# Optimization experiments

Measured on AMD Instinct MI355X. Metric: run time of the kernel, lower is better.

Reference implementation:

```python
import jax, jax.numpy as jnp
import numpy as np

HID, H, C, L = 128, 4, 128, 3  # hidden, heads, per-head out (concat=False -> mean over heads), layers
OUT = 256
N_HEX, N_VERT, N_EDGE, B = 19, 54, 72, 1024
F_HEX, F_VERT, F_EDGE, F_PLY = 9, 7, 5, 14


def _topology():
    # Deterministic stand-in for the Catan board topology (same edge counts as the env).
    rng = np.random.RandomState(0)
    hv = rng.randint(0, N_VERT, size=(N_HEX, 6))            # each hex touches 6 vertices
    v0 = rng.randint(0, N_VERT, size=N_EDGE)                # board-edge endpoints
    v1 = (v0 + 1 + rng.randint(0, N_VERT - 1, size=N_EDGE)) % N_VERT
    h_src = np.repeat(np.arange(N_HEX), 6); h_dst = hv.reshape(-1)           # 114 edges
    e_src = np.repeat(np.arange(N_EDGE), 2); e_dst = np.stack([v0, v1], 1).reshape(-1)  # 144
    vv_s = np.concatenate([v0, v1]); vv_d = np.concatenate([v1, v0])          # 144
    # (src_idx, dst_idx, n_dst) per relation, order matches RELATION_TYPES
    rels = [(h_src, h_dst, N_VERT),   # hex -> vertex
            (h_dst, h_src, N_HEX),    # vertex -> hex
            (e_dst, e_src, N_EDGE),   # vertex -> edge
            (e_src, e_dst, N_VERT),   # edge -> vertex
            (vv_s, vv_d, N_VERT)]     # vertex -> vertex
    return [(jnp.asarray(s, jnp.int32), jnp.asarray(d, jnp.int32), nd) for s, d, nd in rels]

RELS = _topology()
REL_TYPES = [("hex", "vertex"), ("vertex", "hex"), ("vertex", "edge"), ("edge", "vertex"), ("vertex", "vertex")]
NODE_TYPES = ("hex", "vertex", "edge")


def _gat(x_src, x_dst, W, a_s, a_d, b, src, dst, n_dst):
    """PyG GATConv (heads=H, concat=False, add_self_loops=False, shared lin)."""
    bsz = x_src.shape[0]
    g = (x_src @ W).reshape(bsz, -1, H, C)    # [B,Ns,H,C]
    gd = (x_dst @ W).reshape(bsz, -1, H, C)   # [B,Nd,H,C]
    es = jnp.einsum('bnhc,hc->bnh', g, a_s)
    ed = jnp.einsum('bnhc,hc->bnh', gd, a_d)
    e = jax.nn.leaky_relu(es[:, src] + ed[:, dst], 0.2)   # [B,E,H]
    e = jnp.transpose(e, (1, 0, 2))                       # [E,B,H]
    m = jax.ops.segment_max(e, dst, num_segments=n_dst)   # per-dst softmax
    ex = jnp.exp(e - m[dst])
    s = jax.ops.segment_sum(ex, dst, num_segments=n_dst)
    alpha = ex / (s[dst] + 1e-16)
    msg = jnp.transpose(g, (1, 0, 2, 3))[src] * alpha[..., None]   # [E,B,H,C]
    out = jax.ops.segment_sum(msg, dst, num_segments=n_dst)       # [Nd,B,H,C]
    return jnp.transpose(out.mean(axis=2), (1, 0, 2)) + b         # mean over heads, + bias


def _ln(x, g, b):
    mu = x.mean(-1, keepdims=True)
    var = ((x - mu) ** 2).mean(-1, keepdims=True)
    return (x - mu) / jnp.sqrt(var + 1e-5) * g + b


def setup_inputs() -> dict:
    key = jax.random.key(0)
    ks = jax.random.split(key, 20)
    rn = lambda k, shape, s=0.05: jax.random.normal(k, shape, jnp.float32) * s
    pool_dim = 3 * HID + F_PLY
    return {
        'hex_features': rn(ks[0], (B, N_HEX, F_HEX), 1.0),
        'vertex_features': rn(ks[1], (B, N_VERT, F_VERT), 1.0),
        'edge_features': rn(ks[2], (B, N_EDGE, F_EDGE), 1.0),
        'player_features': rn(ks[3], (B, 4, F_PLY), 1.0),
        'in_hexW': rn(ks[4], (F_HEX, HID)), 'in_hexb': jnp.zeros((HID,), jnp.float32),
        'in_vertW': rn(ks[5], (F_VERT, HID)), 'in_vertb': jnp.zeros((HID,), jnp.float32),
        'in_edgeW': rn(ks[6], (F_EDGE, HID)), 'in_edgeb': jnp.zeros((HID,), jnp.float32),
        'gat_W': rn(ks[7], (L, 5, HID, H * C)),
        'gat_asrc': rn(ks[8], (L, 5, H, C)),
        'gat_adst': rn(ks[9], (L, 5, H, C)),
        'gat_b': jnp.zeros((L, 5, C), jnp.float32),
        'ln_g': jnp.ones((L, 3, HID), jnp.float32),
        'ln_b': jnp.zeros((L, 3, HID), jnp.float32),
        'mlp_W1': rn(ks[10], (pool_dim, HID)), 'mlp_b1': jnp.zeros((HID,), jnp.float32),
        'mlp_W2': rn(ks[11], (HID, OUT)), 'mlp_b2': jnp.zeros((OUT,), jnp.float32),
        'current_player': jax.random.randint(ks[12], (B,), 0, 4, jnp.int32),
    }


def reference(hex_features, vertex_features, edge_features, player_features,
              in_hexW, in_hexb, in_vertW, in_vertb, in_edgeW, in_edgeb,
              gat_W, gat_asrc, gat_adst, gat_b, ln_g, ln_b,
              mlp_W1, mlp_b1, mlp_W2, mlp_b2, current_player):
    x = {'hex': hex_features @ in_hexW + in_hexb,
         'vertex': vertex_features @ in_vertW + in_vertb,
         'edge': edge_features @ in_edgeW + in_edgeb}
    for l in range(L):
        agg = {nt: jnp.zeros_like(x[nt]) for nt in NODE_TYPES}
        for r, (st, dt) in enumerate(REL_TYPES):
            src, dst, n_dst = RELS[r]
            agg[dt] = agg[dt] + _gat(x[st], x[dt], gat_W[l, r], gat_asrc[l, r],
                                     gat_adst[l, r], gat_b[l, r], src, dst, n_dst)
        for i, nt in enumerate(NODE_TYPES):
            x[nt] = jax.nn.relu(_ln(agg[nt] + x[nt], ln_g[l, i], ln_b[l, i]))
    pools = [x[nt].mean(axis=1) for nt in NODE_TYPES]  # mean-pool each node type
    cur = jnp.take_along_axis(player_features, current_player[:, None, None], axis=1)[:, 0]
    feat = jnp.concatenate(pools + [cur], axis=-1)     # [B, 3*HID + F_PLY]
    h = jax.nn.relu(feat @ mlp_W1 + mlp_b1)
    return h @ mlp_W2 + mlp_b2
```

## Files before the change

kernel.cpp:

```cpp
#include <hip/hip_runtime.h>
#include <math.h>

#define NB 1024
#define NHEX 19
#define NVERT 54
#define NEDGE 72
#define NNODE 145
#define HID 128
#define NLAYERS 3
#define MAXE 144
#define OUTD 256
#define FPLY 14
#define POOLD 398
#define ESD_PB 5120

typedef unsigned short ushort_t;
typedef short bf16x8 __attribute__((ext_vector_type(8)));
typedef float f32x4 __attribute__((ext_vector_type(4)));
typedef float f32x2 __attribute__((ext_vector_type(2)));

static __device__ __forceinline__ float bf2f(ushort_t u) {
    return __uint_as_float(((unsigned int)u) << 16);
}
static __device__ __forceinline__ ushort_t f2bf(float f) {
    unsigned int u = __float_as_uint(f);
    return (ushort_t)((u + 0x7fffu + ((u >> 16) & 1u)) >> 16);
}
static __device__ __forceinline__ unsigned pk2(float lo, float hi) {
    unsigned r;
    asm("v_cvt_pk_bf16_f32 %0, %1, %2" : "=v"(r) : "v"(lo), "v"(hi));
    return r;
}
static __device__ __forceinline__ float blo(unsigned u) { return __uint_as_float(u << 16); }
static __device__ __forceinline__ float bhi(unsigned u) { return __uint_as_float(u & 0xffff0000u); }
static __device__ __forceinline__ f32x4 MF(uint4 a, uint4 b, f32x4 c) {
    return __builtin_amdgcn_mfma_f32_16x16x32_bf16(
        __builtin_bit_cast(bf16x8, a), __builtin_bit_cast(bf16x8, b), c, 0, 0, 0);
}
static __device__ __forceinline__ int xba(int row, int cb) {
    return (row * 256 + cb) ^ ((row & 7) << 4);
}

__device__ void topo_body(char* sm, int* __restrict__ cst_g, unsigned* __restrict__ pck_g) {
    unsigned* mt = (unsigned*)(sm);
    int* t6   = (int*)(sm + 2496);
    int* sc   = (int*)(sm + 4992);
    int* hv   = (int*)(sm + 7488);
    int* v0a  = (int*)(sm + 7944);
    int* v1a  = (int*)(sm + 8232);
    int* cnt  = (int*)(sm + 8520);
    int* cnt0 = (int*)(sm + 8840);
    int* stt  = (int*)(sm + 9160);
    int* J186 = (int*)(sm + 9480);
    int* M    = (int*)(sm + 9488);
    const int tid = threadIdx.x;

    if (tid == 0) {
        unsigned s = 0u;
        for (int i = 0; i < 624; ++i) { mt[i] = s; s = 1812433253u * (s ^ (s >> 30)) + (unsigned)i + 1u; }
    }
    __syncthreads();
    {
        unsigned a = 0, bb = 0, c = 0;
        if (tid < 227) { a = mt[tid]; bb = mt[tid + 1]; c = mt[tid + 397]; }
        __syncthreads();
        if (tid < 227) {
            unsigned y = (a & 0x80000000u) | (bb & 0x7fffffffu);
            mt[tid] = c ^ (y >> 1) ^ ((bb & 1u) ? 0x9908b0dfu : 0u);
        }
        __syncthreads();
    }
    {
        int i = 227 + tid;
        unsigned a = 0, bb = 0, c = 0;
        if (tid < 227) { a = mt[i]; bb = mt[i + 1]; c = mt[i - 227]; }
        __syncthreads();
        if (tid < 227) {
            unsigned y = (a & 0x80000000u) | (bb & 0x7fffffffu);
            mt[i] = c ^ (y >> 1) ^ ((bb & 1u) ? 0x9908b0dfu : 0u);
        }
        __syncthreads();
    }
    {
        int i = 454 + tid;
        unsigned a = 0, bb = 0, c = 0;
        if (tid < 170) { a = mt[i]; bb = mt[(i + 1) % 624]; c = mt[i - 227]; }
        __syncthreads();
        if (tid < 170) {
            unsigned y = (a & 0x80000000u) | (bb & 0x7fffffffu);
            mt[i] = c ^ (y >> 1) ^ ((bb & 1u) ? 0x9908b0dfu : 0u);
        }
        __syncthreads();
    }
    for (int i = tid; i < 624; i += 256) {
        unsigned y = mt[i];
        y ^= y >> 11; y ^= (y << 7) & 0x9d2c5680u; y ^= (y << 15) & 0xefc60000u; y ^= y >> 18;
        t6[i] = (int)(y & 63u);
    }
    __syncthreads();
#define SCAN624()                                                          \
    for (int off = 1; off < 624; off <<= 1) {                              \
        int v0_ = 0, v1_ = 0, v2_ = 0;                                     \
        int i0 = tid, i1 = tid + 256, i2 = tid + 512;                      \
        if (i0 >= off) v0_ = sc[i0 - off];                                 \
        if (i1 >= off) v1_ = sc[i1 - off];                                 \
        if (i2 < 624 && i2 >= off) v2_ = sc[i2 - off];                     \
        __syncthreads();                                                   \
        sc[i0] += v0_; sc[i1] += v1_;                                      \
        if (i2 < 624) sc[i2] += v2_;                                       \
        __syncthreads();                                                   \
    }
    for (int i = tid; i < 624; i += 256) sc[i] = (t6[i] <= 53) ? 1 : 0;
    __syncthreads();
    SCAN624();
    for (int i = tid; i < 624; i += 256) {
        if (t6[i] <= 53) {
            int k = sc[i];
            if (k <= 114) hv[k - 1] = t6[i];
            else if (k <= 186) v0a[k - 115] = t6[i];
            if (k == 186) *J186 = i;
        }
    }
    __syncthreads();
    int Jcap = *J186;
    for (int i = tid; i < 624; i += 256) sc[i] = (i > Jcap && t6[i] <= 52) ? 1 : 0;
    __syncthreads();
    SCAN624();
    for (int i = tid; i < 624; i += 256) {
        if (i > Jcap && t6[i] <= 52) {
            int k = sc[i];
            if (k <= 72) v1a[k - 1] = (v0a[k - 1] + 1 + t6[i]) % 54;
        }
    }
    __syncthreads();
#undef SCAN624
    const int En[5]  = {114, 114, 144, 144, 144};
    const int Ndn[5] = {54, 19, 72, 54, 54};
    const int Nsn[5] = {19, 54, 54, 72, 54};
    for (int r = 0; r < 5; ++r) {
        const int E = En[r], Nd = Ndn[r], Ns = Nsn[r];
        const int tot = Nd * Ns;
        for (int i = tid; i < tot; i += 256) M[i] = 0;
        __syncthreads();
        for (int k = tid; k < E; k += 256) {
            int s, d;
            if (r == 0)      { s = k / 6; d = hv[k]; }
            else if (r == 1) { s = hv[k]; d = k / 6; }
            else if (r == 2) { s = (k & 1) ? v1a[k >> 1] : v0a[k >> 1]; d = k >> 1; }
            else if (r == 3) { s = k >> 1; d = (k & 1) ? v1a[k >> 1] : v0a[k >> 1]; }
            else             { s = (k < 72) ? v0a[k] : v1a[k - 72]; d = (k < 72) ? v1a[k] : v0a[k - 72]; }
            atomicAdd(&M[d * Ns + s], 1);
        }
        __syncthreads();
        if (tid < Nd) {
            int c = 0;
            const int base = tid * Ns;
            for (int s = 0; s < Ns; ++s) c += (M[base + s] != 0) ? 1 : 0;
            cnt[tid] = c;
            cnt0[tid] = c;
        }
        __syncthreads();
        for (int off = 1; off < 128; off <<= 1) {
            int v = 0;
            if (tid < Nd && tid >= off) v = cnt[tid - off];
            __syncthreads();
            if (tid < Nd && tid >= off) cnt[tid] += v;
            __syncthreads();
        }
        if (tid < Nd) {
            int st = cnt[tid] - cnt0[tid];
            stt[tid] = st;
            cst_g[r * 73 + tid] = st;
            if (tid == Nd - 1) cst_g[r * 73 + Nd] = cnt[tid];
        }
        __syncthreads();
        for (int i = tid; i < tot; i += 256) {
            int m = M[i];
            if (m > 0) {
                int d = i / Ns, s = i - d * Ns;
                int rank = 0;
                const int base = d * Ns;
                for (int s2 = 0; s2 < s; ++s2) rank += (M[base + s2] != 0) ? 1 : 0;
                pck_g[r * 144 + stt[d] + rank] = (unsigned)(s | (d << 8) | (m << 16));
            }
        }
        __syncthreads();
    }
}

__device__ void wvec_body(char* sm, int lr, const float* __restrict__ gat_W,
                          const float* __restrict__ gat_asrc,
                          const float* __restrict__ gat_adst,
                          ushort_t* __restrict__ wvb) {
    float* as_s = (float*)(sm);
    float* ad_s = (float*)(sm + 2048);
    int tid = threadIdx.x;
    for (int i = tid; i < 512; i += 256) {
        as_s[i] = gat_asrc[(size_t)lr * 512 + i];
        ad_s[i] = gat_adst[(size_t)lr * 512 + i];
    }
    __syncthreads();
    ushort_t* wb = wvb + (size_t)lr * 2048;
    const float* W = gat_W + (size_t)lr * 128 * 512;
    int t127 = tid & 127, rhalf = tid >> 7;
    int h = t127 >> 5, c4 = t127 & 31;
    for (int k0 = 0; k0 < 128; k0 += 2) {
        int k = k0 + rhalf;
        float4 wv4 = *(const float4*)(W + (size_t)k * 512 + h * 128 + c4 * 4);
        const float* a = as_s + h * 128 + c4 * 4;
        const float* dd = ad_s + h * 128 + c4 * 4;
        float pa = wv4.x * a[0] + wv4.y * a[1] + wv4.z * a[2] + wv4.w * a[3];
        float pd = wv4.x * dd[0] + wv4.y * dd[1] + wv4.z * dd[2] + wv4.w * dd[3];
        for (int m = 1; m < 32; m <<= 1) { pa += __shfl_xor(pa, m, 64); pd += __shfl_xor(pd, m, 64); }
        if (c4 == 0) {
            ushort_t pah = f2bf(pa), pdh = f2bf(pd);
            ushort_t pal = f2bf(pa - bf2f(pah)), pdl = f2bf(pd - bf2f(pdh));
            wb[h * 128 + k] = pah;        wb[(4 + h) * 128 + k] = pdh;
            wb[(8 + h) * 128 + k] = pal;  wb[(12 + h) * 128 + k] = pdl;
        }
    }
}

__device__ void wp_body(char* sm, int lrh, const float* __restrict__ gat_W, ushort_t* __restrict__ Wp) {
    ushort_t* tr = (ushort_t*)(sm);
    int lr = lrh >> 2, h = lrh & 3;
    const float* Wsrc = gat_W + (size_t)lr * 128 * 512 + h * 128;
    ushort_t* dst = Wp + (size_t)lrh * 128 * 128;
    for (int half = 0; half < 2; ++half) {
        for (int i = threadIdx.x; i < 128 * 16; i += 256) {
            int k = i >> 4, q2 = i & 15;
            float4 v = *(const float4*)(Wsrc + (size_t)k * 512 + half * 64 + q2 * 4);
            int nl = q2 * 4;
            tr[(nl + 0) * 130 + k] = f2bf(v.x);
            tr[(nl + 1) * 130 + k] = f2bf(v.y);
            tr[(nl + 2) * 130 + k] = f2bf(v.z);
            tr[(nl + 3) * 130 + k] = f2bf(v.w);
        }
        __syncthreads();
        for (int i = threadIdx.x; i < 64 * 16; i += 256) {
            int nl = i >> 4, q = i & 15;
            const ushort_t* s = tr + nl * 130 + q * 8;
            uint4 o;
            o.x = (unsigned)s[0] | ((unsigned)s[1] << 16);
            o.y = (unsigned)s[2] | ((unsigned)s[3] << 16);
            o.z = (unsigned)s[4] | ((unsigned)s[5] << 16);
            o.w = (unsigned)s[6] | ((unsigned)s[7] << 16);
            *(uint4*)(dst + (half * 64 + nl) * 128 + q * 8) = o;
        }
        __syncthreads();
    }
}

__global__ __launch_bounds__(256) void k_preA(
        int* __restrict__ cst_g, unsigned* __restrict__ pck_g,
        const float* __restrict__ gatW, const float* __restrict__ gatas,
        const float* __restrict__ gatad, ushort_t* __restrict__ wvb, ushort_t* __restrict__ Wp) {
    extern __shared__ char smem_dyn[];
    unsigned kb = blockIdx.x;
    if (kb == 0)      topo_body(smem_dyn, cst_g, pck_g);
    else if (kb < 16) wvec_body(smem_dyn, (int)kb - 1, gatW, gatas, gatad, wvb);
    else              wp_body(smem_dyn, (int)kb - 16, gatW, Wp);
}
#define PREA_SMEM 25088

__global__ __launch_bounds__(256) void k_projlog(
        const float* __restrict__ hexf, const float* __restrict__ vertf,
        const float* __restrict__ edgef,
        const float* __restrict__ Wh, const float* __restrict__ bh,
        const float* __restrict__ Wv, const float* __restrict__ bv,
        const float* __restrict__ We, const float* __restrict__ be,
        ushort_t* __restrict__ xb, const ushort_t* __restrict__ wvb,
        float* __restrict__ esd_g) {
    extern __shared__ char smem_dyn[];
    char*  smem = smem_dyn;
    float* Wl = (float*)(smem + 37120);
    float* bl = (float*)(smem + 48384);
    int b = blockIdx.x, tid = threadIdx.x, lane = tid & 63, wid = tid >> 6;
    const int kc16 = (lane >> 4) * 16;

    for (int i = tid; i < 9 * 128; i += 256) Wl[i] = Wh[i];
    for (int i = tid; i < 7 * 128; i += 256) Wl[9 * 128 + i] = Wv[i];
    for (int i = tid; i < 5 * 128; i += 256) Wl[16 * 128 + i] = We[i];
    if (tid < 128) { bl[tid] = bh[tid]; bl[128 + tid] = bv[tid]; bl[256 + tid] = be[tid]; }
    __syncthreads();
    int c = tid & 127;
    for (int n = tid >> 7; n < NNODE; n += 2) {
        const float* f; const float* W; const float* bias; int K;
        if (n < NHEX)              { f = hexf  + ((size_t)b * NHEX  + n) * 9;                  W = Wl;            bias = bl;       K = 9; }
        else if (n < NHEX + NVERT) { f = vertf + ((size_t)b * NVERT + (n - NHEX)) * 7;         W = Wl + 9 * 128;  bias = bl + 128; K = 7; }
        else                       { f = edgef + ((size_t)b * NEDGE + (n - NHEX - NVERT)) * 5; W = Wl + 16 * 128; bias = bl + 256; K = 5; }
        float acc = bias[c];
        for (int k = 0; k < K; ++k) acc += f[k] * W[k * 128 + c];
        ushort_t u = f2bf(acc);
        xb[((size_t)b * NNODE + n) * HID + c] = u;
        *(ushort_t*)(smem + xba(n, c * 2)) = u;
    }
    __syncthreads();

    const int NsA[5] = {19, 54, 54, 72, 54}, SbA[5] = {0, 19, 19, 73, 19};
    const int NdA[5] = {54, 19, 72, 54, 54}, DbA[5] = {19, 0, 73, 19, 19};
    for (int r = 0; r < 5; ++r) {
        int Ns = NsA[r];
        int RL = (r == 4) ? 54 : Ns + NdA[r];
        const ushort_t* wv = wvb + (size_t)r * 2048;
        uint4 bw[4];
#pragma unroll
        for (int ks = 0; ks < 4; ++ks)
            bw[ks] = *(const uint4*)(wv + (lane & 15) * 128 + ks * 32 + (lane >> 4) * 8);
        int T = (RL + 15) >> 4;
        for (int t = wid; t < T; t += 4) {
            int vrow = t * 16 + (lane & 15);
            int node = vrow < Ns ? SbA[r] + vrow : (vrow < RL ? DbA[r] + (vrow - Ns) : SbA[r]);
            f32x4 e = (f32x4){0.f, 0.f, 0.f, 0.f};
#pragma unroll
            for (int ks = 0; ks < 4; ++ks)
                e = MF(*(const uint4*)(smem + xba(node, ks * 64 + kc16)), bw[ks], e);
#pragma unroll
            for (int g = 0; g < 4; ++g) {
                float sv = e[g] + __shfl_xor(e[g], 8, 64);
                int row = t * 16 + (lane >> 4) * 4 + g;
                if ((lane & 15) < 8 && row < RL)
                    esd_g[(size_t)b * ESD_PB + r * 1024 + row * 8 + (lane & 15)] = sv;
            }
        }
    }
}
#define PROJLOG_SMEM 49920

template<int KIND>
__device__ __forceinline__ void gnn_body(char* smem, int b, int half,
        const ushort_t* __restrict__ xb_cur, ushort_t* __restrict__ xb_nxt,
        const float* __restrict__ esd_cur, float* __restrict__ esd_nxt,
        const int* __restrict__ cst_all, const unsigned* __restrict__ pck_all,
        const ushort_t* __restrict__ wvb, const ushort_t* __restrict__ Wp_g,
        const float* __restrict__ gatb_g,
        const float* __restrict__ lg, const float* __restrict__ lb, int l) {
    constexpr int ND    = (KIND == 0 ? 19 : KIND == 1 ? 36 : 54);
    constexpr int DBASE = (KIND == 0 ? 0 : KIND == 1 ? 73 : 19);
    constexpr int NSMAX = (KIND == 2 ? 72 : 54);
    constexpr int NRELF = (KIND == 2 ? 3 : 1);
    constexpr int MT    = (ND + 15) / 16;
    constexpr int O_Y   = NSMAX * 256;
    constexpr int O_ESD = O_Y + ND * 256;
    constexpr int O_AL  = O_ESD + 4064;
    constexpr int O_CST = O_AL + 2304;
    constexpr int O_PCK = O_CST + 304;

    constexpr int NS_A[3][3] = {{54, 0, 0}, {54, 0, 0}, {19, 72, 54}};
    constexpr int SB_A[3][3] = {{19, 0, 0}, {19, 0, 0}, {0, 73, 19}};
    constexpr int RR_A[3][3] = {{1, 0, 0}, {2, 0, 0}, {0, 3, 4}};
    constexpr int NRE = (KIND == 2 ? 5 : 2);
    constexpr int RE_R[3][5] = {{0, 1, 0, 0, 0}, {2, 3, 0, 0, 0}, {0, 1, 2, 3, 4}};
    constexpr int RE_B[3][5] = {{0, 54, 0, 0, 0}, {54, 0, 0, 0, 0}, {19, 0, 0, 72, 0}};

    float*    esdL = (float*)(smem + O_ESD);
    float*    alph = (float*)(smem + O_AL);
    int*      cstL = (int*)(smem + O_CST);
    unsigned* pckL = (unsigned*)(smem + O_PCK);

    const int tid = threadIdx.x, lane = tid & 63, wid = tid >> 6;
    const int nr0 = wid * 32 + (lane & 15);
    const int kc16 = (lane >> 4) * 16;
    const int d0 = half * ND;
    const int DB = DBASE + d0;
    const ushort_t* xcb = xb_cur + (size_t)b * NNODE * HID;

    f32x4 acc[MT][2];
#pragma unroll
    for (int mt = 0; mt < MT; ++mt) {
        acc[mt][0] = (f32x4){0.f, 0.f, 0.f, 0.f};
        acc[mt][1] = (f32x4){0.f, 0.f, 0.f, 0.f};
    }

#pragma unroll
    for (int ri = 0; ri < NRELF; ++ri) {
        const int NS = NS_A[KIND][ri], SBG = SB_A[KIND][ri], r = RR_A[KIND][ri];
        const bool SELF = (KIND == 2 && ri == 2);
        const int lr = l * 5 + r;
        const int ER = SELF ? ND : NS + ND;
        const int jlo = cst_all[r * 73 + d0];

        for (int i = tid; i < NS * 16; i += 256) {
            int row = i >> 4, q = i & 15;
            uint4 o = *(const uint4*)(xcb + (size_t)(SBG + row) * HID + q * 8);
            *(uint4*)(smem + xba(row, q * 16)) = o;
        }
        {
            const float* eg = esd_cur + (size_t)b * ESD_PB + (size_t)r * 1024;
            for (int i = tid; i < ER * 2; i += 256) {
                int row = i >> 1;
                int grow = (SELF || row < NS) ? row : row + d0;
                ((uint4*)esdL)[i] = ((const uint4*)eg)[grow * 2 + (i & 1)];
            }
        }
        for (int i = tid; i <= ND; i += 256) cstL[i] = cst_all[r * 73 + d0 + i] - jlo;
        for (int i = tid; jlo + i < 144; i += 256) pckL[i] = pck_all[r * 144 + jlo + i];
        __syncthreads();

        for (int i = tid; i < ND * 4; i += 256) {
            int d = i >> 2, h = i & 3;
            int s0 = cstL[d], s1 = cstL[d + 1];
            if (s0 == s1) continue;
            float edv = esdL[((SELF ? d + d0 : NS + d)) * 8 + 4 + h];
            float m = -1e30f;
            for (int j = s0; j < s1; ++j) {
                float sv = esdL[(pckL[j] & 255) * 8 + h] + edv;
                sv = (sv >= 0.f) ? sv : 0.2f * sv;
                alph[j * 4 + h] = sv;
                m = fmaxf(m, sv);
            }
            float sum = 0.f;
            for (int j = s0; j < s1; ++j) {
                float e = (float)(pckL[j] >> 16) * __expf(alph[j * 4 + h] - m);
                alph[j * 4 + h] = e;
                sum += e;
            }
            float inv = 1.f / (sum + 1e-16f);
            for (int j = s0; j < s1; ++j) alph[j * 4 + h] *= inv;
        }
        __syncthreads();

        for (int h = 0; h < 4; ++h) {
            for (int i = tid; i < ND * 16; i += 256) {
                int d = i >> 4, c8 = i & 15;
                int s0 = cstL[d], s1 = cstL[d + 1];
                f32x2 a01 = (f32x2){0.f, 0.f}, a23 = (f32x2){0.f, 0.f};
                f32x2 a45 = (f32x2){0.f, 0.f}, a67 = (f32x2){0.f, 0.f};
                for (int j = s0; j < s1; ++j) {
                    float al = alph[j * 4 + h];
                    f32x2 al2 = (f32x2){al, al};
                    uint4 xv = *(const uint4*)(smem + xba((int)(pckL[j] & 255), c8 * 16));
                    a01 += al2 * (f32x2){blo(xv.x), bhi(xv.x)};
                    a23 += al2 * (f32x2){blo(xv.y), bhi(xv.y)};
                    a45 += al2 * (f32x2){blo(xv.z), bhi(xv.z)};
                    a67 += al2 * (f32x2){blo(xv.w), bhi(xv.w)};
                }
                uint4 o;
                o.x = pk2(a01[0], a01[1]); o.y = pk2(a23[0], a23[1]);
                o.z = pk2(a45[0], a45[1]); o.w = pk2(a67[0], a67[1]);
                *(uint4*)(smem + O_Y + xba(d, c8 * 16)) = o;
            }
            const ushort_t* wpH = Wp_g + (size_t)(lr * 4 + h) * 16384;
            __syncthreads();
#pragma unroll
            for (int ks = 0; ks < 4; ++ks) {
                uint4 b0 = *(const uint4*)(wpH + (size_t)nr0 * 128 + ks * 32 + (lane >> 4) * 8);
                uint4 b1 = *(const uint4*)(wpH + (size_t)(nr0 + 16) * 128 + ks * 32 + (lane >> 4) * 8);
#pragma unroll
                for (int mt = 0; mt < MT; ++mt) {
                    int arow = mt * 16 + (lane & 15);
                    if (arow >= ND) arow = ND - 1;
                    uint4 av = *(const uint4*)(smem + O_Y + xba(arow, ks * 64 + kc16));
                    acc[mt][0] = MF(av, b0, acc[mt][0]);
                    acc[mt][1] = MF(av, b1, acc[mt][1]);
                }
            }
            __syncthreads();
        }
    }

    float bn0 = 0.f, bn1 = 0.f;
#pragma unroll
    for (int ri = 0; ri < NRELF; ++ri) {
        const float* bb = gatb_g + (size_t)(l * 5 + RR_A[KIND][ri]) * 128;
        bn0 += bb[nr0]; bn1 += bb[nr0 + 16];
    }
    const float lgc0 = lg[nr0], lgc1 = lg[nr0 + 16];
    const float lbc0 = lb[nr0], lbc1 = lb[nr0 + 16];
#pragma unroll
    for (int mt = 0; mt < MT; ++mt)
#pragma unroll
        for (int g = 0; g < 4; ++g) {
            int row = mt * 16 + (lane >> 4) * 4 + g;
            if (row < ND) {
                acc[mt][0][g] = 0.25f * acc[mt][0][g] + bn0 + bf2f(xcb[(size_t)(DB + row) * HID + nr0]);
                acc[mt][1][g] = 0.25f * acc[mt][1][g] + bn1 + bf2f(xcb[(size_t)(DB + row) * HID + nr0 + 16]);
            }
        }
    float* red1 = esdL;
    float* red2 = esdL + 320;
#pragma unroll
    for (int mt = 0; mt < MT; ++mt)
#pragma unroll
        for (int g = 0; g < 4; ++g) {
            float p = acc[mt][0][g] + acc[mt][1][g];
            for (int m = 1; m < 16; m <<= 1) p += __shfl_xor(p, m, 64);
            int row = mt * 16 + (lane >> 4) * 4 + g;
            if ((lane & 15) == 0 && row < ND) red1[row * 4 + wid] = p;
        }
    __syncthreads();
#pragma unroll
    for (int mt = 0; mt < MT; ++mt)
#pragma unroll
        for (int g = 0; g < 4; ++g) {
            int row = mt * 16 + (lane >> 4) * 4 + g;
            float mu = 0.f;
            if (row < ND)
                mu = (red1[row * 4] + red1[row * 4 + 1] + red1[row * 4 + 2] + red1[row * 4 + 3]) * (1.f / 128.f);
            acc[mt][0][g] -= mu;
            acc[mt][1][g] -= mu;
            float p = acc[mt][0][g] * acc[mt][0][g] + acc[mt][1][g] * acc[mt][1][g];
            for (int m = 1; m < 16; m <<= 1) p += __shfl_xor(p, m, 64);
            if ((lane & 15) == 0 && row < ND) red2[row * 4 + wid] = p;
        }
    __syncthreads();
#pragma unroll
    for (int mt = 0; mt < MT; ++mt)
#pragma unroll
        for (int g = 0; g < 4; ++g) {
            int row = mt * 16 + (lane >> 4) * 4 + g;
            if (row < ND) {
                float var = (red2[row * 4] + red2[row * 4 + 1] + red2[row * 4 + 2] + red2[row * 4 + 3]) * (1.f / 128.f);
                float rs = rsqrtf(var + 1e-5f);
                float o0 = fmaxf(acc[mt][0][g] * rs * lgc0 + lbc0, 0.f);
                float o1 = fmaxf(acc[mt][1][g] * rs * lgc1 + lbc1, 0.f);
                size_t gi = ((size_t)b * NNODE + DB + row) * HID;
                ushort_t u0 = f2bf(o0), u1 = f2bf(o1);
                xb_nxt[gi + nr0] = u0;
                xb_nxt[gi + nr0 + 16] = u1;
                if (esd_nxt) {
                    *(ushort_t*)(smem + O_Y + xba(row, nr0 * 2)) = u0;
                    *(ushort_t*)(smem + O_Y + xba(row, (nr0 + 16) * 2)) = u1;
                }
            }
        }
    if (esd_nxt) {
        __syncthreads();
        const int T = (ND + 15) >> 4;
        for (int t5 = wid; t5 < NRE * T; t5 += 4) {
            int e = t5 / T, tt = t5 % T;
            int r2 = RE_R[KIND][e], base = RE_B[KIND][e] + d0;
            const ushort_t* wv = wvb + (size_t)((l + 1) * 5 + r2) * 2048;
            uint4 bw[4];
#pragma unroll
            for (int ks = 0; ks < 4; ++ks)
                bw[ks] = *(const uint4*)(wv + (lane & 15) * 128 + ks * 32 + (lane >> 4) * 8);
            int arow = tt * 16 + (lane & 15);
            if (arow >= ND) arow = ND - 1;
            f32x4 ev = (f32x4){0.f, 0.f, 0.f, 0.f};
#pragma unroll
            for (int ks = 0; ks < 4; ++ks)
                ev = MF(*(const uint4*)(smem + O_Y + xba(arow, ks * 64 + kc16)), bw[ks], ev);
#pragma unroll
            for (int g = 0; g < 4; ++g) {
                float sv = ev[g] + __shfl_xor(ev[g], 8, 64);
                int row = tt * 16 + (lane >> 4) * 4 + g;
                if ((lane & 15) < 8 && row < ND)
                    esd_nxt[(size_t)b * ESD_PB + r2 * 1024 + (base + row) * 8 + (lane & 15)] = sv;
            }
        }
    }
}

#define SMEM_TOT 39504

__global__ __launch_bounds__(256, 4) void k_layer(
        const ushort_t* __restrict__ xb_cur, ushort_t* __restrict__ xb_nxt,
        const float* __restrict__ esd_cur, float* __restrict__ esd_nxt,
        const int* __restrict__ cst, const unsigned* __restrict__ pck,
        const ushort_t* __restrict__ wvb, const ushort_t* __restrict__ Wp,
        const float* __restrict__ gatb, const float* __restrict__ lngp,
        const float* __restrict__ lnbp, int l) {
    extern __shared__ uint4 smem_u4[];
    char* smem = (char*)smem_u4;
    unsigned kb = blockIdx.x;
    if (kb < NB)
        gnn_body<2>(smem, (int)kb, 0, xb_cur, xb_nxt, esd_cur, esd_nxt, cst, pck, wvb, Wp, gatb,
                    lngp + (size_t)(l * 3 + 1) * 128, lnbp + (size_t)(l * 3 + 1) * 128, l);
    else if (kb < 3 * NB) {
        unsigned t = kb - NB;
        gnn_body<1>(smem, (int)(t >> 1), (int)(t & 1), xb_cur, xb_nxt, esd_cur, esd_nxt, cst, pck, wvb, Wp, gatb,
                    lngp + (size_t)(l * 3 + 2) * 128, lnbp + (size_t)(l * 3 + 2) * 128, l);
    } else
        gnn_body<0>(smem, (int)(kb - 3 * NB), 0, xb_cur, xb_nxt, esd_cur, esd_nxt, cst, pck, wvb, Wp, gatb,
                    lngp + (size_t)(l * 3 + 0) * 128, lnbp + (size_t)(l * 3 + 0) * 128, l);
}

__global__ __launch_bounds__(256) void k_head(const ushort_t* __restrict__ xb, const float* __restrict__ playerf,
                                              const int* __restrict__ curp,
                                              const float* __restrict__ W1, const float* __restrict__ b1,
                                              const float* __restrict__ W2, const float* __restrict__ b2,
                                              float* __restrict__ out) {
    __shared__ float fs[POOLD];
    __shared__ float ps[256];
    __shared__ float h1s[HID];
    int b = blockIdx.x, t = threadIdx.x;
    int c = t & 127, half = t >> 7;
    const ushort_t* xbb = xb + (size_t)b * NNODE * HID;
    float s0 = 0.f, s1 = 0.f, s2 = 0.f;
    for (int n = half; n < NHEX; n += 2)                    s0 += bf2f(xbb[n * HID + c]);
    for (int n = NHEX + half; n < NHEX + NVERT; n += 2)     s1 += bf2f(xbb[n * HID + c]);
    for (int n = NHEX + NVERT + half; n < NNODE; n += 2)    s2 += bf2f(xbb[n * HID + c]);
    ps[t] = s0; __syncthreads();
    if (half == 0) fs[c] = (ps[c] + ps[128 + c]) * (1.f / 19.f);
    __syncthreads(); ps[t] = s1; __syncthreads();
    if (half == 0) fs[128 + c] = (ps[c] + ps[128 + c]) * (1.f / 54.f);
    __syncthreads(); ps[t] = s2; __syncthreads();
    if (half == 0) fs[256 + c] = (ps[c] + ps[128 + c]) * (1.f / 72.f);
    if (t < FPLY) fs[384 + t] = playerf[((size_t)b * 4 + curp[b]) * FPLY + t];
    __syncthreads();
    float a = 0.f;
    int k0 = half * 199, k1 = half ? POOLD : 199;
    for (int k = k0; k < k1; ++k) a += fs[k] * W1[(size_t)k * HID + c];
    ps[t] = a; __syncthreads();
    if (half == 0) h1s[c] = fmaxf(b1[c] + ps[c] + ps[128 + c], 0.f);
    __syncthreads();
    float o = b2[t];
    for (int j = 0; j < HID; ++j) o += h1s[j] * W2[(size_t)j * OUTD + t];
    out[(size_t)b * OUTD + t] = o;
}

static constexpr size_t alignUp(size_t v) { return (v + 255) & ~(size_t)255; }
static constexpr size_t OFF_CST  = 0;
static constexpr size_t OFF_PCK  = alignUp(OFF_CST + 5 * 73 * 4);
static constexpr size_t OFF_WVB  = alignUp(OFF_PCK + 5 * 144 * 4);
static constexpr size_t OFF_WP   = alignUp(OFF_WVB + (size_t)15 * 16 * 128 * 2);
static constexpr size_t OFF_XA   = alignUp(OFF_WP + (size_t)15 * 4 * 128 * 128 * 2);
static constexpr size_t OFF_XB2  = alignUp(OFF_XA + (size_t)NB * NNODE * HID * 2);
static constexpr size_t OFF_ESD0 = alignUp(OFF_XB2 + (size_t)NB * NNODE * HID * 2);
static constexpr size_t OFF_ESD1 = alignUp(OFF_ESD0 + (size_t)NB * ESD_PB * 4);

extern "C" void kernel_launch(void* const* d_in, const int* in_sizes, int n_in,
                              void* d_out, int out_size, void* d_ws, size_t ws_size,
                              hipStream_t stream) {
    (void)in_sizes; (void)n_in; (void)out_size; (void)ws_size;
    const float* hexf   = (const float*)d_in[0];
    const float* vertf  = (const float*)d_in[1];
    const float* edgef  = (const float*)d_in[2];
    const float* playerf= (const float*)d_in[3];
    const float* inhW   = (const float*)d_in[4];
    const float* inhb   = (const float*)d_in[5];
    const float* invW   = (const float*)d_in[6];
    const float* invb   = (const float*)d_in[7];
    const float* ineW   = (const float*)d_in[8];
    const float* ineb   = (const float*)d_in[9];
    const float* gatW   = (const float*)d_in[10];
    const float* gatas  = (const float*)d_in[11];
    const float* gatad  = (const float*)d_in[12];
    const float* gatb   = (const float*)d_in[13];
    const float* lngp   = (const float*)d_in[14];
    const float* lnbp   = (const float*)d_in[15];
    const float* mW1    = (const float*)d_in[16];
    const float* mb1    = (const float*)d_in[17];
    const float* mW2    = (const float*)d_in[18];
    const float* mb2    = (const float*)d_in[19];
    const int*   curp   = (const int*)d_in[20];
    float* out = (float*)d_out;

    char* ws = (char*)d_ws;
    int* cst        = (int*)(ws + OFF_CST);
    unsigned* pck   = (unsigned*)(ws + OFF_PCK);
    ushort_t* wvb   = (ushort_t*)(ws + OFF_WVB);
    ushort_t* Wp    = (ushort_t*)(ws + OFF_WP);
    ushort_t* xbA   = (ushort_t*)(ws + OFF_XA);
    ushort_t* xbB   = (ushort_t*)(ws + OFF_XB2);
    float* esd0     = (float*)(ws + OFF_ESD0);
    float* esd1     = (float*)(ws + OFF_ESD1);

    k_preA<<<76, 256, PREA_SMEM, stream>>>(cst, pck, gatW, gatas, gatad, wvb, Wp);
    k_projlog<<<NB, 256, PROJLOG_SMEM, stream>>>(hexf, vertf, edgef, inhW, inhb, invW, invb,
                                                 ineW, ineb, xbA, wvb, esd0);

    for (int l = 0; l < NLAYERS; ++l) {
        const ushort_t* cur = (l & 1) ? xbB : xbA;
        ushort_t* nxt = (l & 1) ? xbA : xbB;
        const float* ecur = (l & 1) ? esd1 : esd0;
        float* enxt = (l == 2) ? nullptr : ((l & 1) ? esd0 : esd1);
        k_layer<<<4 * NB, 256, SMEM_TOT, stream>>>(cur, nxt, ecur, enxt, cst, pck, wvb, Wp,
                                                   gatb, lngp, lnbp, l);
    }

    k_head<<<NB, 256, 0, stream>>>(xbB, playerf, curp, mW1, mb1, mW2, mb2, out);
}
```

Baseline: 779.9 us.

## Split vertex blocks in half and process two attention heads per pass

Vertex-destination work is split across two blocks of 27 nodes each, growing the grid from 4*NB to 5*NB blocks. The head loop now aggregates two heads per pass into two Y buffers, halving the number of syncthreads and aggregation passes while doubling the MFMA work per pass. Launch bounds drop from 4 to 2 waves per SIMD, which gives the extra accumulators more registers but may lower occupancy. The shared-memory layout grows because of the second Y buffer. The self-relation ESD row count changes to NS so that all 54 source rows are loaded.

```diff
diff --git a/kernel.cpp b/kernel.cpp
--- a/kernel.cpp
+++ b/kernel.cpp
@@ -335,13 +335,14 @@
         const ushort_t* __restrict__ wvb, const ushort_t* __restrict__ Wp_g,
         const float* __restrict__ gatb_g,
         const float* __restrict__ lg, const float* __restrict__ lb, int l) {
-    constexpr int ND    = (KIND == 0 ? 19 : KIND == 1 ? 36 : 54);
+    constexpr int ND    = (KIND == 0 ? 19 : KIND == 1 ? 36 : 27);
     constexpr int DBASE = (KIND == 0 ? 0 : KIND == 1 ? 73 : 19);
     constexpr int NSMAX = (KIND == 2 ? 72 : 54);
     constexpr int NRELF = (KIND == 2 ? 3 : 1);
     constexpr int MT    = (ND + 15) / 16;
     constexpr int O_Y   = NSMAX * 256;
-    constexpr int O_ESD = O_Y + ND * 256;
+    constexpr int YB1   = ND * 256;
+    constexpr int O_ESD = O_Y + 2 * ND * 256;
     constexpr int O_AL  = O_ESD + 4064;
     constexpr int O_CST = O_AL + 2304;
     constexpr int O_PCK = O_CST + 304;
@@ -377,7 +378,7 @@
         const int NS = NS_A[KIND][ri], SBG = SB_A[KIND][ri], r = RR_A[KIND][ri];
         const bool SELF = (KIND == 2 && ri == 2);
         const int lr = l * 5 + r;
-        const int ER = SELF ? ND : NS + ND;
+        const int ER = SELF ? NS : NS + ND;
         const int jlo = cst_all[r * 73 + d0];
 
         for (int i = tid; i < NS * 16; i += 256) {
@@ -420,39 +421,57 @@
         }
         __syncthreads();
 
-        for (int h = 0; h < 4; ++h) {
+#pragma unroll
+        for (int hp = 0; hp < 2; ++hp) {
+            const int h0 = hp * 2;
             for (int i = tid; i < ND * 16; i += 256) {
                 int d = i >> 4, c8 = i & 15;
                 int s0 = cstL[d], s1 = cstL[d + 1];
-                f32x2 a01 = (f32x2){0.f, 0.f}, a23 = (f32x2){0.f, 0.f};
-                f32x2 a45 = (f32x2){0.f, 0.f}, a67 = (f32x2){0.f, 0.f};
+                f32x2 y0a = (f32x2){0.f, 0.f}, y0b = (f32x2){0.f, 0.f};
+                f32x2 y0c = (f32x2){0.f, 0.f}, y0d = (f32x2){0.f, 0.f};
+                f32x2 y1a = (f32x2){0.f, 0.f}, y1b = (f32x2){0.f, 0.f};
+                f32x2 y1c = (f32x2){0.f, 0.f}, y1d = (f32x2){0.f, 0.f};
                 for (int j = s0; j < s1; ++j) {
-                    float al = alph[j * 4 + h];
-                    f32x2 al2 = (f32x2){al, al};
+                    float al0 = alph[j * 4 + h0];
+                    float al1 = alph[j * 4 + h0 + 1];
+                    f32x2 v0 = (f32x2){al0, al0}, v1 = (f32x2){al1, al1};
                     uint4 xv = *(const uint4*)(smem + xba((int)(pckL[j] & 255), c8 * 16));
-                    a01 += al2 * (f32x2){blo(xv.x), bhi(xv.x)};
-                    a23 += al2 * (f32x2){blo(xv.y), bhi(xv.y)};
-                    a45 += al2 * (f32x2){blo(xv.z), bhi(xv.z)};
-                    a67 += al2 * (f32x2){blo(xv.w), bhi(xv.w)};
+                    f32x2 e0 = (f32x2){blo(xv.x), bhi(xv.x)};
+                    f32x2 e1 = (f32x2){blo(xv.y), bhi(xv.y)};
+                    f32x2 e2 = (f32x2){blo(xv.z), bhi(xv.z)};
+                    f32x2 e3 = (f32x2){blo(xv.w), bhi(xv.w)};
+                    y0a += v0 * e0; y0b += v0 * e1; y0c += v0 * e2; y0d += v0 * e3;
+                    y1a += v1 * e0; y1b += v1 * e1; y1c += v1 * e2; y1d += v1 * e3;
                 }
-                uint4 o;
-                o.x = pk2(a01[0], a01[1]); o.y = pk2(a23[0], a23[1]);
-                o.z = pk2(a45[0], a45[1]); o.w = pk2(a67[0], a67[1]);
-                *(uint4*)(smem + O_Y + xba(d, c8 * 16)) = o;
-            }
-            const ushort_t* wpH = Wp_g + (size_t)(lr * 4 + h) * 16384;
+                uint4 o0, o1;
+                o0.x = pk2(y0a[0], y0a[1]); o0.y = pk2(y0b[0], y0b[1]);
+                o0.z = pk2(y0c[0], y0c[1]); o0.w = pk2(y0d[0], y0d[1]);
+                o1.x = pk2(y1a[0], y1a[1]); o1.y = pk2(y1b[0], y1b[1]);
+                o1.z = pk2(y1c[0], y1c[1]); o1.w = pk2(y1d[0], y1d[1]);
+                int ba = xba(d, c8 * 16);
+                *(uint4*)(smem + O_Y + ba) = o0;
+                *(uint4*)(smem + O_Y + YB1 + ba) = o1;
+            }
+            const ushort_t* wpH0 = Wp_g + (size_t)(lr * 4 + h0) * 16384;
+            const ushort_t* wpH1 = wpH0 + 16384;
             __syncthreads();
 #pragma unroll
             for (int ks = 0; ks < 4; ++ks) {
-                uint4 b0 = *(const uint4*)(wpH + (size_t)nr0 * 128 + ks * 32 + (lane >> 4) * 8);
-                uint4 b1 = *(const uint4*)(wpH + (size_t)(nr0 + 16) * 128 + ks * 32 + (lane >> 4) * 8);
+                uint4 b00 = *(const uint4*)(wpH0 + (size_t)nr0 * 128 + ks * 32 + (lane >> 4) * 8);
+                uint4 b01 = *(const uint4*)(wpH0 + (size_t)(nr0 + 16) * 128 + ks * 32 + (lane >> 4) * 8);
+                uint4 b10 = *(const uint4*)(wpH1 + (size_t)nr0 * 128 + ks * 32 + (lane >> 4) * 8);
+                uint4 b11 = *(const uint4*)(wpH1 + (size_t)(nr0 + 16) * 128 + ks * 32 + (lane >> 4) * 8);
 #pragma unroll
                 for (int mt = 0; mt < MT; ++mt) {
                     int arow = mt * 16 + (lane & 15);
                     if (arow >= ND) arow = ND - 1;
-                    uint4 av = *(const uint4*)(smem + O_Y + xba(arow, ks * 64 + kc16));
-                    acc[mt][0] = MF(av, b0, acc[mt][0]);
-                    acc[mt][1] = MF(av, b1, acc[mt][1]);
+                    int ba = xba(arow, ks * 64 + kc16);
+                    uint4 av0 = *(const uint4*)(smem + O_Y + ba);
+                    uint4 av1 = *(const uint4*)(smem + O_Y + YB1 + ba);
+                    acc[mt][0] = MF(av0, b00, acc[mt][0]);
+                    acc[mt][1] = MF(av0, b01, acc[mt][1]);
+                    acc[mt][0] = MF(av1, b10, acc[mt][0]);
+                    acc[mt][1] = MF(av1, b11, acc[mt][1]);
                 }
             }
             __syncthreads();
@@ -554,7 +573,7 @@
 
 #define SMEM_TOT 39504
 
-__global__ __launch_bounds__(256, 4) void k_layer(
+__global__ __launch_bounds__(256, 2) void k_layer(
         const ushort_t* __restrict__ xb_cur, ushort_t* __restrict__ xb_nxt,
         const float* __restrict__ esd_cur, float* __restrict__ esd_nxt,
         const int* __restrict__ cst, const unsigned* __restrict__ pck,
@@ -564,15 +583,15 @@
     extern __shared__ uint4 smem_u4[];
     char* smem = (char*)smem_u4;
     unsigned kb = blockIdx.x;
-    if (kb < NB)
-        gnn_body<2>(smem, (int)kb, 0, xb_cur, xb_nxt, esd_cur, esd_nxt, cst, pck, wvb, Wp, gatb,
+    if (kb < 2 * NB)
+        gnn_body<2>(smem, (int)(kb >> 1), (int)(kb & 1), xb_cur, xb_nxt, esd_cur, esd_nxt, cst, pck, wvb, Wp, gatb,
                     lngp + (size_t)(l * 3 + 1) * 128, lnbp + (size_t)(l * 3 + 1) * 128, l);
-    else if (kb < 3 * NB) {
-        unsigned t = kb - NB;
+    else if (kb < 4 * NB) {
+        unsigned t = kb - 2 * NB;
         gnn_body<1>(smem, (int)(t >> 1), (int)(t & 1), xb_cur, xb_nxt, esd_cur, esd_nxt, cst, pck, wvb, Wp, gatb,
                     lngp + (size_t)(l * 3 + 2) * 128, lnbp + (size_t)(l * 3 + 2) * 128, l);
     } else
-        gnn_body<0>(smem, (int)(kb - 3 * NB), 0, xb_cur, xb_nxt, esd_cur, esd_nxt, cst, pck, wvb, Wp, gatb,
+        gnn_body<0>(smem, (int)(kb - 4 * NB), 0, xb_cur, xb_nxt, esd_cur, esd_nxt, cst, pck, wvb, Wp, gatb,
                     lngp + (size_t)(l * 3 + 0) * 128, lnbp + (size_t)(l * 3 + 0) * 128, l);
 }
 
@@ -666,7 +685,7 @@
         ushort_t* nxt = (l & 1) ? xbA : xbB;
         const float* ecur = (l & 1) ? esd1 : esd0;
         float* enxt = (l == 2) ? nullptr : ((l & 1) ? esd0 : esd1);
-        k_layer<<<4 * NB, 256, SMEM_TOT, stream>>>(cur, nxt, ecur, enxt, cst, pck, wvb, Wp,
+        k_layer<<<5 * NB, 256, SMEM_TOT, stream>>>(cur, nxt, ecur, enxt, cst, pck, wvb, Wp,
                                                    gatb, lngp, lnbp, l);
     }
 
```

Measured after the change: 1.002 ms. +28.5%, slower.
